# Performance work log

Hardware: AMD Instinct MI355X
Metric: run time of the kernel (lower is better)

## Reference

```python
import jax, jax.numpy as jnp
import numpy as np

BN_EPS = 1e-5
L2_EPS = 1e-12


def setup_inputs() -> dict:
    key = jax.random.key(0)
    k1, k2, k3 = jax.random.split(key, 3)
    B, N, D, K, G = 32, 2048, 512, 64, 16
    init_sc = 1.0 / np.sqrt(D)
    x = jax.random.normal(k1, (B, N, D), dtype=jnp.float32)
    clusters = init_sc * jax.random.normal(k2, (D, K + G), dtype=jnp.float32)
    clusters2 = init_sc * jax.random.normal(k3, (1, D, K), dtype=jnp.float32)
    bn_gamma = jnp.ones((K + G,), dtype=jnp.float32)
    bn_beta = jnp.zeros((K + G,), dtype=jnp.float32)
    return {"x": x, "clusters": clusters, "clusters2": clusters2,
            "bn_gamma": bn_gamma, "bn_beta": bn_beta}


def reference(x, clusters, clusters2, bn_gamma, bn_beta):
    B, N, D = x.shape
    K = clusters2.shape[-1]
    xf = x.reshape(B * N, D)
    # soft cluster assignment: [B*N, K+G]
    assn = xf @ clusters
    # BatchNorm1d (training-mode batch statistics, biased variance)
    mean = jnp.mean(assn, axis=0)
    var = jnp.var(assn, axis=0)
    assn = (assn - mean) * jax.lax.rsqrt(var + BN_EPS) * bn_gamma + bn_beta
    # softmax over clusters, then drop ghost clusters
    assn = jax.nn.softmax(assn, axis=1)[:, :K].reshape(B, N, K)
    # residual aggregation
    a_sum = jnp.sum(assn, axis=1, keepdims=True)          # [B, 1, K]
    a = a_sum * clusters2                                  # [B, D, K]
    vlad = jnp.einsum("bnk,bnd->bdk", assn, x) - a         # [B, D, K]
    # intra-normalization across feature dim D
    vlad = vlad / jnp.maximum(jnp.linalg.norm(vlad, axis=1, keepdims=True), L2_EPS)
    # flatten and global L2 normalization
    vlad = vlad.reshape(B, D * K)
    vlad = vlad / jnp.maximum(jnp.linalg.norm(vlad, axis=1, keepdims=True), L2_EPS)
    return vlad
```

## Files before the change

### kernel.cpp

```cpp
#include <hip/hip_runtime.h>
#include <hip/hip_bf16.h>
#include <stdint.h>

typedef __attribute__((ext_vector_type(8))) short short8;
typedef __attribute__((ext_vector_type(4))) float f32x4;

__device__ __forceinline__ float b2f(uint16_t u) {
  union { uint32_t i; float f; } v; v.i = ((uint32_t)u) << 16; return v.f;
}
__device__ __forceinline__ uint16_t f2b(float f) {
  uint32_t u = __float_as_uint(f);
  return (uint16_t)((u + 0x7FFFu + ((u >> 16) & 1u)) >> 16);
}
__device__ __forceinline__ uint32_t pk2(uint32_t lo, uint32_t hi) {
  return __builtin_amdgcn_perm(hi + 0x8000u, lo + 0x8000u, 0x07060302u);
}

__global__ void k0_prep(const float* __restrict__ clusters,
                        uint16_t* __restrict__ cB) {
  int gid = blockIdx.x * 256 + threadIdx.x;
  if (gid < 40960) {
    int i = gid & 7, chunk = gid >> 3;
    int lr = chunk & 15, q = (chunk >> 4) & 3, c5 = chunk >> 6;
    int n = c5 % 5, kk = c5 / 5;
    cB[gid] = f2b(clusters[(kk * 32 + q * 8 + i) * 80 + n * 16 + lr]);
  }
}

__global__ __launch_bounds__(256) void k1_gemm1(
    const float* __restrict__ x, const uint16_t* __restrict__ cB,
    float* __restrict__ raw, float* __restrict__ part) {
  __shared__ __align__(16) uint16_t lB[80 * 256];
  const int t = threadIdx.x;
  const int w = t >> 6, lane = t & 63, q = lane >> 4, lr = lane & 15;
  const int rbase = blockIdx.x * 128 + w * 32;

  f32x4 acc[2][5];
#pragma unroll
  for (int m = 0; m < 2; ++m)
#pragma unroll
    for (int n = 0; n < 5; ++n) acc[m][n] = 0.f;

  const float* xa = x + (size_t)(rbase + lr) * 512 + q * 8;

  for (int h = 0; h < 2; ++h) {
    if (h) __syncthreads();
#pragma unroll 2
    for (int idx = t; idx < 2560; idx += 256)
      *(uint4*)&lB[idx * 8] = ((const uint4*)cB)[h * 2560 + idx];
    __syncthreads();
#pragma unroll
    for (int kk8 = 0; kk8 < 8; ++kk8) {
      const int kk = h * 8 + kk8;
      short8 a[2], bf[5];
#pragma unroll
      for (int m = 0; m < 2; ++m) {
        uint4 u0 = *(const uint4*)(xa + (size_t)m * 16 * 512 + kk * 32);
        uint4 u1 = *(const uint4*)(xa + (size_t)m * 16 * 512 + kk * 32 + 4);
        union { short8 s; uint32_t u[4]; } av;
        av.u[0] = pk2(u0.x, u0.y); av.u[1] = pk2(u0.z, u0.w);
        av.u[2] = pk2(u1.x, u1.y); av.u[3] = pk2(u1.z, u1.w);
        a[m] = av.s;
      }
#pragma unroll
      for (int n = 0; n < 5; ++n)
        bf[n] = *(const short8*)&lB[(((kk8 * 5 + n) * 4 + q) * 16 + lr) * 8];
#pragma unroll
      for (int m = 0; m < 2; ++m)
#pragma unroll
        for (int n = 0; n < 5; ++n)
          acc[m][n] = __builtin_amdgcn_mfma_f32_16x16x32_bf16(a[m], bf[n], acc[m][n], 0, 0, 0);
    }
  }
  __syncthreads();

  float sums[5], sqs[5];
#pragma unroll
  for (int n = 0; n < 5; ++n) {
    float s = 0.f, qq = 0.f;
#pragma unroll
    for (int m = 0; m < 2; ++m) {
#pragma unroll
      for (int r = 0; r < 4; ++r) {
        float v = acc[m][n][r];
        s += v; qq += v * v;
        raw[(size_t)(rbase + m * 16 + q * 4 + r) * 80 + n * 16 + lr] = v;
      }
    }
    s += __shfl_xor(s, 16);  s += __shfl_xor(s, 32);
    qq += __shfl_xor(qq, 16); qq += __shfl_xor(qq, 32);
    sums[n] = s; sqs[n] = qq;
  }

  float* sf = (float*)lB;
  if (lane < 16) {
#pragma unroll
    for (int n = 0; n < 5; ++n) {
      sf[w * 160 + n * 16 + lr] = sums[n];
      sf[640 + w * 160 + n * 16 + lr] = sqs[n];
    }
  }
  __syncthreads();
  if (t < 160) {
    float a0 = sf[t] + sf[160 + t] + sf[320 + t] + sf[480 + t];
    float b0 = sf[640 + t] + sf[800 + t] + sf[960 + t] + sf[1120 + t];
    part[(size_t)blockIdx.x * 320 + t] = a0;
    part[(size_t)blockIdx.x * 320 + 160 + t] = b0;
  }
}

__global__ __launch_bounds__(64) void k2_stats(
    const float* __restrict__ part, const float* __restrict__ gamma,
    const float* __restrict__ beta, float* __restrict__ scsh,
    float* __restrict__ a_sum) {
  int c = blockIdx.x, t = threadIdx.x;
  int gid = c * 64 + t;
  if (gid < 2048) a_sum[gid] = 0.f;
  float s1 = 0.f, s2 = 0.f;
  for (int p = t; p < 512; p += 64) {
    s1 += part[(size_t)p * 320 + c];
    s2 += part[(size_t)p * 320 + 160 + c];
  }
#pragma unroll
  for (int o = 1; o < 64; o <<= 1) { s1 += __shfl_xor(s1, o); s2 += __shfl_xor(s2, o); }
  if (t == 0) {
    float mean = s1 * (1.f / 65536.f);
    float var = s2 * (1.f / 65536.f) - mean * mean;
    float sc = rsqrtf(var + 1e-5f) * gamma[c];
    scsh[c] = sc;
    scsh[80 + c] = beta[c] - mean * sc;
  }
}

__global__ __launch_bounds__(256) void k3_bnsoft(
    const float* __restrict__ raw, const float* __restrict__ scsh,
    uint16_t* __restrict__ pT, float* __restrict__ a_sum) {
  __shared__ float sc[80], sh[80];
  __shared__ __align__(16) uint16_t lpT[64 * 72];
  __shared__ float apart[256];
  const int t = threadIdx.x;
  if (t < 80) sc[t] = scsh[t];
  else if (t < 160) sh[t - 80] = scsh[t];
  __syncthreads();

  const int r = t >> 2, cg = t & 3;
  const float* rp = raw + ((size_t)blockIdx.x * 64 + r) * 80;
  const int cbase = cg * 20;

  float y[20];
#pragma unroll
  for (int j = 0; j < 20; j += 4) {
    float4 v = *(const float4*)(rp + cbase + j);
    y[j] = v.x; y[j + 1] = v.y; y[j + 2] = v.z; y[j + 3] = v.w;
  }
  float mx = -3.0e38f;
#pragma unroll
  for (int j = 0; j < 20; ++j) {
    int c = cbase + j;
    y[j] = y[j] * sc[c] + sh[c];
    mx = fmaxf(mx, y[j]);
  }
  mx = fmaxf(mx, __shfl_xor(mx, 1));
  mx = fmaxf(mx, __shfl_xor(mx, 2));
  float sum = 0.f;
#pragma unroll
  for (int j = 0; j < 20; ++j) { y[j] = __expf(y[j] - mx); sum += y[j]; }
  sum += __shfl_xor(sum, 1);
  sum += __shfl_xor(sum, 2);
  float inv = 1.0f / sum;
#pragma unroll
  for (int j = 0; j < 20; ++j) {
    int c = cbase + j;
    if (c < 64) lpT[c * 72 + r] = f2b(y[j] * inv);
  }
  __syncthreads();

  {
    int k = t >> 2, ng = t & 3;
    uint4 v0 = *(const uint4*)&lpT[k * 72 + ng * 16];
    uint4 v1 = *(const uint4*)&lpT[k * 72 + ng * 16 + 8];
    int b = blockIdx.x >> 5;
    int n0 = (blockIdx.x & 31) * 64;
    uint16_t* dst = pT + ((size_t)b * 64 + k) * 2048 + n0 + ng * 16;
    *(uint4*)dst = v0;
    *((uint4*)dst + 1) = v1;
    const uint16_t* pv = &lpT[k * 72 + ng * 16];
    float s = 0.f;
#pragma unroll
    for (int i = 0; i < 16; ++i) s += b2f(pv[i]);
    apart[k * 4 + ng] = s;
  }
  __syncthreads();
  if (t < 64) {
    float s = apart[t * 4] + apart[t * 4 + 1] + apart[t * 4 + 2] + apart[t * 4 + 3];
    atomicAdd(&a_sum[(blockIdx.x >> 5) * 64 + t], s);
  }
}

__global__ __launch_bounds__(256) void k4_gemm2(
    const float* __restrict__ x, const uint16_t* __restrict__ pT,
    float* __restrict__ vpart) {
  __shared__ __align__(16) uint16_t sx[2][64 * 40];
  __shared__ __align__(16) uint16_t sp[2][64 * 40];
  const int t = threadIdx.x;
  const int nb = blockIdx.x >> 8;
  const int b = (blockIdx.x >> 3) & 31;
  const int d0 = (blockIdx.x & 7) * 64;
  const int w = t >> 6, lane = t & 63, q = lane >> 4, lr = lane & 15;
  const int dl = w * 16 + lr;
  const int sw = ((dl >> 2) + (dl >> 4)) & 3;

  const int dd = t & 63, g = t >> 6;
  const int sg = ((dd >> 2) + (dd >> 4)) & 3;
  const int pk_ = t >> 2, pnq = t & 3;

  const float* xb = x + ((size_t)b * 2048 + (size_t)nb * 1024) * 512 + d0;
  const uint16_t* pb = pT + (size_t)b * 131072 + (size_t)nb * 1024;

  f32x4 acc[4];
#pragma unroll
  for (int j = 0; j < 4; ++j) acc[j] = 0.f;

  float xf[2][8];
  uint4 pf[2];

#define LOADC(c, si)                                                        \
  {                                                                         \
    const float* xc = xb + (size_t)(c) * 32 * 512;                          \
    _Pragma("unroll")                                                       \
    for (int jj = 0; jj < 8; ++jj)                                          \
      xf[si][jj] = xc[(size_t)(g * 8 + jj) * 512 + dd];                     \
    pf[si] = *(const uint4*)(pb + (size_t)pk_ * 2048 + (c) * 32 + pnq * 8); \
  }
#define STOREC(buf, si)                                                     \
  {                                                                         \
    uint16_t* xrow = &sx[buf][dd * 40 + (g ^ sg) * 8];                      \
    _Pragma("unroll")                                                       \
    for (int j = 0; j < 2; ++j) {                                           \
      *(uint32_t*)&xrow[j * 4] =                                            \
          pk2(__float_as_uint(xf[si][j * 4]), __float_as_uint(xf[si][j * 4 + 1])); \
      *(uint32_t*)&xrow[j * 4 + 2] =                                        \
          pk2(__float_as_uint(xf[si][j * 4 + 2]), __float_as_uint(xf[si][j * 4 + 3])); \
    }                                                                       \
    *(uint4*)&sp[buf][pk_ * 40 + pnq * 8] = pf[si];                         \
  }

  LOADC(0, 0)
  STOREC(0, 0)
  LOADC(1, 1)
  __syncthreads();

  for (int c = 0; c < 32; ++c) {
    const int cur = c & 1;
    if (c < 31) STOREC(cur ^ 1, (c + 1) & 1)
    if (c < 30) LOADC(c + 2, c & 1)
    const uint16_t* sxc = sx[cur];
    const uint16_t* spc = sp[cur];
    short8 af = *(const short8*)&sxc[dl * 40 + (q ^ sw) * 8];
#pragma unroll
    for (int j = 0; j < 4; ++j) {
      short8 bfj = *(const short8*)&spc[(j * 16 + lr) * 40 + q * 8];
      acc[j] = __builtin_amdgcn_mfma_f32_16x16x32_bf16(af, bfj, acc[j], 0, 0, 0);
    }
    __syncthreads();
  }
#undef LOADC
#undef STOREC

  float* vp = vpart + (size_t)nb * 1048576 + (size_t)b * 32768;
#pragma unroll
  for (int j = 0; j < 4; ++j)
#pragma unroll
    for (int r = 0; r < 4; ++r)
      vp[(size_t)(d0 + w * 16 + q * 4 + r) * 64 + j * 16 + lr] = acc[j][r];
}

__global__ __launch_bounds__(256) void k5a_ssq(
    const float* __restrict__ vpart, const float* __restrict__ a_sum,
    const float* __restrict__ c2, float* __restrict__ csq) {
  __shared__ float sred[256];
  const int t = threadIdx.x, b = blockIdx.x >> 4, dg = blockIdx.x & 15;
  const int k = t & 63, di = t >> 6;
  const float* v0 = vpart + (size_t)b * 32768;
  const float* v1 = v0 + 1048576;
  const float as = a_sum[b * 64 + k];
  float ssq = 0.f;
#pragma unroll
  for (int jj = 0; jj < 8; ++jj) {
    int i = (dg * 32 + di * 8 + jj) * 64 + k;
    float v = v0[i] + v1[i] - as * c2[i];
    ssq += v * v;
  }
  sred[di * 64 + k] = ssq;
  __syncthreads();
  if (t < 64) {
    csq[(size_t)blockIdx.x * 64 + t] =
        sred[t] + sred[64 + t] + sred[128 + t] + sred[192 + t];
  }
}

__global__ __launch_bounds__(64) void k5b_fin(
    const float* __restrict__ csq, float* __restrict__ linv,
    float* __restrict__ gscl) {
  const int t = threadIdx.x, b = blockIdx.x;
  float ssq = 0.f;
#pragma unroll
  for (int dg = 0; dg < 16; ++dg) ssq += csq[(size_t)(b * 16 + dg) * 64 + t];
  float iv = 1.0f / fmaxf(sqrtf(ssq), 1e-12f);
  linv[b * 64 + t] = iv;
  float contrib = ssq * iv * iv;
#pragma unroll
  for (int o = 1; o < 64; o <<= 1) contrib += __shfl_xor(contrib, o);
  if (t == 0) gscl[b] = 1.0f / fmaxf(sqrtf(contrib), 1e-12f);
}

__global__ __launch_bounds__(256) void k5c_norm(
    const float* __restrict__ vpart, const float* __restrict__ a_sum,
    const float* __restrict__ c2, const float* __restrict__ linv,
    const float* __restrict__ gscl, float* __restrict__ out) {
  __shared__ float lv[64], las[64];
  __shared__ float gs;
  const int t = threadIdx.x, b = blockIdx.x >> 4, seg = blockIdx.x & 15;
  if (t < 64) { lv[t] = linv[b * 64 + t]; las[t] = a_sum[b * 64 + t]; }
  if (t == 64) gs = gscl[b];
  __syncthreads();
  const float* v0 = vpart + (size_t)b * 32768;
  const float* v1 = v0 + 1048576;
  const float gg = gs;
#pragma unroll
  for (int u = 0; u < 2; ++u) {
    int i = seg * 2048 + u * 1024 + t * 4;
    int k0 = i & 63;
    float4 a = *(const float4*)(v0 + i);
    float4 bb = *(const float4*)(v1 + i);
    float4 cc = *(const float4*)(c2 + i);
    float4 o;
    o.x = (a.x + bb.x - las[k0 + 0] * cc.x) * lv[k0 + 0] * gg;
    o.y = (a.y + bb.y - las[k0 + 1] * cc.y) * lv[k0 + 1] * gg;
    o.z = (a.z + bb.z - las[k0 + 2] * cc.z) * lv[k0 + 2] * gg;
    o.w = (a.w + bb.w - las[k0 + 3] * cc.w) * lv[k0 + 3] * gg;
    *(float4*)&out[(size_t)b * 32768 + i] = o;
  }
}

extern "C" void kernel_launch(void* const* d_in, const int* in_sizes, int n_in,
                              void* d_out, int out_size, void* d_ws, size_t ws_size,
                              hipStream_t stream) {
  const float* x         = (const float*)d_in[0];
  const float* clusters  = (const float*)d_in[1];
  const float* clusters2 = (const float*)d_in[2];
  const float* gamma     = (const float*)d_in[3];
  const float* beta      = (const float*)d_in[4];
  float* out = (float*)d_out;
  char* ws = (char*)d_ws;

  uint16_t* cB = (uint16_t*)(ws + 0);
  float* part  = (float*)(ws + 81920);
  float* scsh  = (float*)(ws + 737280);
  float* a_sum = (float*)(ws + 737920);
  float* raw   = (float*)(ws + 746112);
  uint16_t* pT = (uint16_t*)(ws + 21717632);
  float* vpart = (float*)(ws + 30106240);
  float* csq   = (float*)(ws + 38494848);
  float* linv  = (float*)(ws + 38625920);
  float* gscl  = (float*)(ws + 38634112);

  hipLaunchKernelGGL(k0_prep,   dim3(160), dim3(256), 0, stream, clusters, cB);
  hipLaunchKernelGGL(k1_gemm1,  dim3(512), dim3(256), 0, stream, x, cB, raw, part);
  hipLaunchKernelGGL(k2_stats,  dim3(80),  dim3(64),  0, stream, part, gamma, beta, scsh, a_sum);
  hipLaunchKernelGGL(k3_bnsoft, dim3(1024),dim3(256), 0, stream, raw, scsh, pT, a_sum);
  hipLaunchKernelGGL(k4_gemm2,  dim3(512), dim3(256), 0, stream, x, pT, vpart);
  hipLaunchKernelGGL(k5a_ssq,   dim3(512), dim3(256), 0, stream, vpart, a_sum, clusters2, csq);
  hipLaunchKernelGGL(k5b_fin,   dim3(32),  dim3(64),  0, stream, csq, linv, gscl);
  hipLaunchKernelGGL(k5c_norm,  dim3(512), dim3(256), 0, stream, vpart, a_sum, clusters2, linv, gscl, out);
}
```

Baseline: 257.9 us.

## Fuse BN-softmax into second GEMM and restructure reduction pipeline

Merges the batchnorm/softmax kernel with the aggregation GEMM, so softmax probabilities are computed per tile straight into shared memory instead of being written out as a transposed bf16 buffer and read back. The GEMM now splits N into 8 segments with larger 256-wide D tiles, and a new reduction kernel sums the 8 partial results into a full buffer. The cluster-sum atomics are replaced by per-segment partials. The first GEMM loads all of cB into LDS once, and the stats partials are transposed so reads are coalesced. The cost is a larger vpart (8 partials) and an extra vfull write/read.

```diff
diff --git a/kernel.cpp b/kernel.cpp
--- a/kernel.cpp
+++ b/kernel.cpp
@@ -30,11 +30,18 @@
 __global__ __launch_bounds__(256) void k1_gemm1(
     const float* __restrict__ x, const uint16_t* __restrict__ cB,
     float* __restrict__ raw, float* __restrict__ part) {
-  __shared__ __align__(16) uint16_t lB[80 * 256];
+  __shared__ __align__(16) uint16_t lB[80 * 512];
   const int t = threadIdx.x;
   const int w = t >> 6, lane = t & 63, q = lane >> 4, lr = lane & 15;
   const int rbase = blockIdx.x * 128 + w * 32;
 
+  {
+    const uint4* src = (const uint4*)cB;
+#pragma unroll 4
+    for (int it = 0; it < 20; ++it)
+      *(uint4*)&lB[(it * 256 + t) * 8] = src[it * 256 + t];
+  }
+
   f32x4 acc[2][5];
 #pragma unroll
   for (int m = 0; m < 2; ++m)
@@ -42,35 +49,28 @@
     for (int n = 0; n < 5; ++n) acc[m][n] = 0.f;
 
   const float* xa = x + (size_t)(rbase + lr) * 512 + q * 8;
-
-  for (int h = 0; h < 2; ++h) {
-    if (h) __syncthreads();
-#pragma unroll 2
-    for (int idx = t; idx < 2560; idx += 256)
-      *(uint4*)&lB[idx * 8] = ((const uint4*)cB)[h * 2560 + idx];
-    __syncthreads();
-#pragma unroll
-    for (int kk8 = 0; kk8 < 8; ++kk8) {
-      const int kk = h * 8 + kk8;
-      short8 a[2], bf[5];
-#pragma unroll
-      for (int m = 0; m < 2; ++m) {
-        uint4 u0 = *(const uint4*)(xa + (size_t)m * 16 * 512 + kk * 32);
-        uint4 u1 = *(const uint4*)(xa + (size_t)m * 16 * 512 + kk * 32 + 4);
-        union { short8 s; uint32_t u[4]; } av;
-        av.u[0] = pk2(u0.x, u0.y); av.u[1] = pk2(u0.z, u0.w);
-        av.u[2] = pk2(u1.x, u1.y); av.u[3] = pk2(u1.z, u1.w);
-        a[m] = av.s;
-      }
+  __syncthreads();
+
+#pragma unroll 8
+  for (int kk = 0; kk < 16; ++kk) {
+    short8 a[2], bf[5];
+#pragma unroll
+    for (int m = 0; m < 2; ++m) {
+      uint4 u0 = *(const uint4*)(xa + (size_t)m * 16 * 512 + kk * 32);
+      uint4 u1 = *(const uint4*)(xa + (size_t)m * 16 * 512 + kk * 32 + 4);
+      union { short8 s; uint32_t u[4]; } av;
+      av.u[0] = pk2(u0.x, u0.y); av.u[1] = pk2(u0.z, u0.w);
+      av.u[2] = pk2(u1.x, u1.y); av.u[3] = pk2(u1.z, u1.w);
+      a[m] = av.s;
+    }
+#pragma unroll
+    for (int n = 0; n < 5; ++n)
+      bf[n] = *(const short8*)&lB[(((kk * 5 + n) * 4 + q) * 16 + lr) * 8];
+#pragma unroll
+    for (int m = 0; m < 2; ++m)
 #pragma unroll
       for (int n = 0; n < 5; ++n)
-        bf[n] = *(const short8*)&lB[(((kk8 * 5 + n) * 4 + q) * 16 + lr) * 8];
-#pragma unroll
-      for (int m = 0; m < 2; ++m)
-#pragma unroll
-        for (int n = 0; n < 5; ++n)
-          acc[m][n] = __builtin_amdgcn_mfma_f32_16x16x32_bf16(a[m], bf[n], acc[m][n], 0, 0, 0);
-    }
+        acc[m][n] = __builtin_amdgcn_mfma_f32_16x16x32_bf16(a[m], bf[n], acc[m][n], 0, 0, 0);
   }
   __syncthreads();
 
@@ -104,23 +104,20 @@
   if (t < 160) {
     float a0 = sf[t] + sf[160 + t] + sf[320 + t] + sf[480 + t];
     float b0 = sf[640 + t] + sf[800 + t] + sf[960 + t] + sf[1120 + t];
-    part[(size_t)blockIdx.x * 320 + t] = a0;
-    part[(size_t)blockIdx.x * 320 + 160 + t] = b0;
+    part[(size_t)t * 512 + blockIdx.x] = a0;
+    part[(size_t)(160 + t) * 512 + blockIdx.x] = b0;
   }
 }
 
 __global__ __launch_bounds__(64) void k2_stats(
     const float* __restrict__ part, const float* __restrict__ gamma,
-    const float* __restrict__ beta, float* __restrict__ scsh,
-    float* __restrict__ a_sum) {
+    const float* __restrict__ beta, float* __restrict__ scsh) {
   int c = blockIdx.x, t = threadIdx.x;
-  int gid = c * 64 + t;
-  if (gid < 2048) a_sum[gid] = 0.f;
+  const float* p1 = part + (size_t)c * 512;
+  const float* p2 = part + (size_t)(160 + c) * 512;
   float s1 = 0.f, s2 = 0.f;
-  for (int p = t; p < 512; p += 64) {
-    s1 += part[(size_t)p * 320 + c];
-    s2 += part[(size_t)p * 320 + 160 + c];
-  }
+#pragma unroll
+  for (int p = 0; p < 512; p += 64) { s1 += p1[p + t]; s2 += p2[p + t]; }
 #pragma unroll
   for (int o = 1; o < 64; o <<= 1) { s1 += __shfl_xor(s1, o); s2 += __shfl_xor(s2, o); }
   if (t == 0) {
@@ -132,163 +129,180 @@
   }
 }
 
-__global__ __launch_bounds__(256) void k3_bnsoft(
-    const float* __restrict__ raw, const float* __restrict__ scsh,
-    uint16_t* __restrict__ pT, float* __restrict__ a_sum) {
+__global__ __launch_bounds__(256, 2) void k34_fused(
+    const float* __restrict__ x, const float* __restrict__ raw_,
+    const float* __restrict__ scsh, float* __restrict__ vpart,
+    float* __restrict__ apart) {
+  __shared__ __align__(16) uint16_t sx[2][256 * 40];
+  __shared__ __align__(16) uint16_t sp[2][64 * 40];
   __shared__ float sc[80], sh[80];
-  __shared__ __align__(16) uint16_t lpT[64 * 72];
-  __shared__ float apart[256];
+  __shared__ float ared[4 * 64];
+
   const int t = threadIdx.x;
+  const int b = blockIdx.x >> 4;
+  const int s = (blockIdx.x >> 1) & 7;
+  const int dh = blockIdx.x & 1;
+  const int w = t >> 6, lane = t & 63, q = lane >> 4, lr = lane & 15;
+
+  const int dd = t;
+  const int sg = ((dd >> 2) + (dd >> 4)) & 3;
+  const int r_ = t >> 3, cg = t & 7;
+  const int kk_ = t & 63, ng = t >> 6;
+
   if (t < 80) sc[t] = scsh[t];
   else if (t < 160) sh[t - 80] = scsh[t];
-  __syncthreads();
-
-  const int r = t >> 2, cg = t & 3;
-  const float* rp = raw + ((size_t)blockIdx.x * 64 + r) * 80;
-  const int cbase = cg * 20;
-
-  float y[20];
-#pragma unroll
-  for (int j = 0; j < 20; j += 4) {
-    float4 v = *(const float4*)(rp + cbase + j);
-    y[j] = v.x; y[j + 1] = v.y; y[j + 2] = v.z; y[j + 3] = v.w;
-  }
-  float mx = -3.0e38f;
-#pragma unroll
-  for (int j = 0; j < 20; ++j) {
-    int c = cbase + j;
-    y[j] = y[j] * sc[c] + sh[c];
-    mx = fmaxf(mx, y[j]);
-  }
-  mx = fmaxf(mx, __shfl_xor(mx, 1));
-  mx = fmaxf(mx, __shfl_xor(mx, 2));
-  float sum = 0.f;
-#pragma unroll
-  for (int j = 0; j < 20; ++j) { y[j] = __expf(y[j] - mx); sum += y[j]; }
-  sum += __shfl_xor(sum, 1);
-  sum += __shfl_xor(sum, 2);
-  float inv = 1.0f / sum;
-#pragma unroll
-  for (int j = 0; j < 20; ++j) {
-    int c = cbase + j;
-    if (c < 64) lpT[c * 72 + r] = f2b(y[j] * inv);
-  }
-  __syncthreads();
-
-  {
-    int k = t >> 2, ng = t & 3;
-    uint4 v0 = *(const uint4*)&lpT[k * 72 + ng * 16];
-    uint4 v1 = *(const uint4*)&lpT[k * 72 + ng * 16 + 8];
-    int b = blockIdx.x >> 5;
-    int n0 = (blockIdx.x & 31) * 64;
-    uint16_t* dst = pT + ((size_t)b * 64 + k) * 2048 + n0 + ng * 16;
-    *(uint4*)dst = v0;
-    *((uint4*)dst + 1) = v1;
-    const uint16_t* pv = &lpT[k * 72 + ng * 16];
-    float s = 0.f;
-#pragma unroll
-    for (int i = 0; i < 16; ++i) s += b2f(pv[i]);
-    apart[k * 4 + ng] = s;
-  }
-  __syncthreads();
-  if (t < 64) {
-    float s = apart[t * 4] + apart[t * 4 + 1] + apart[t * 4 + 2] + apart[t * 4 + 3];
-    atomicAdd(&a_sum[(blockIdx.x >> 5) * 64 + t], s);
-  }
-}
-
-__global__ __launch_bounds__(256) void k4_gemm2(
-    const float* __restrict__ x, const uint16_t* __restrict__ pT,
-    float* __restrict__ vpart) {
-  __shared__ __align__(16) uint16_t sx[2][64 * 40];
-  __shared__ __align__(16) uint16_t sp[2][64 * 40];
-  const int t = threadIdx.x;
-  const int nb = blockIdx.x >> 8;
-  const int b = (blockIdx.x >> 3) & 31;
-  const int d0 = (blockIdx.x & 7) * 64;
-  const int w = t >> 6, lane = t & 63, q = lane >> 4, lr = lane & 15;
-  const int dl = w * 16 + lr;
-  const int sw = ((dl >> 2) + (dl >> 4)) & 3;
-
-  const int dd = t & 63, g = t >> 6;
-  const int sg = ((dd >> 2) + (dd >> 4)) & 3;
-  const int pk_ = t >> 2, pnq = t & 3;
-
-  const float* xb = x + ((size_t)b * 2048 + (size_t)nb * 1024) * 512 + d0;
-  const uint16_t* pb = pT + (size_t)b * 131072 + (size_t)nb * 1024;
-
-  f32x4 acc[4];
-#pragma unroll
-  for (int j = 0; j < 4; ++j) acc[j] = 0.f;
-
-  float xf[2][8];
-  uint4 pf[2];
-
-#define LOADC(c, si)                                                        \
-  {                                                                         \
-    const float* xc = xb + (size_t)(c) * 32 * 512;                          \
-    _Pragma("unroll")                                                       \
-    for (int jj = 0; jj < 8; ++jj)                                          \
-      xf[si][jj] = xc[(size_t)(g * 8 + jj) * 512 + dd];                     \
-    pf[si] = *(const uint4*)(pb + (size_t)pk_ * 2048 + (c) * 32 + pnq * 8); \
-  }
-#define STOREC(buf, si)                                                     \
-  {                                                                         \
-    uint16_t* xrow = &sx[buf][dd * 40 + (g ^ sg) * 8];                      \
-    _Pragma("unroll")                                                       \
-    for (int j = 0; j < 2; ++j) {                                           \
-      *(uint32_t*)&xrow[j * 4] =                                            \
-          pk2(__float_as_uint(xf[si][j * 4]), __float_as_uint(xf[si][j * 4 + 1])); \
-      *(uint32_t*)&xrow[j * 4 + 2] =                                        \
-          pk2(__float_as_uint(xf[si][j * 4 + 2]), __float_as_uint(xf[si][j * 4 + 3])); \
-    }                                                                       \
-    *(uint4*)&sp[buf][pk_ * 40 + pnq * 8] = pf[si];                         \
-  }
-
-  LOADC(0, 0)
-  STOREC(0, 0)
-  LOADC(1, 1)
-  __syncthreads();
-
-  for (int c = 0; c < 32; ++c) {
+
+  const float* xb = x + ((size_t)b * 2048 + (size_t)s * 256) * 512 + dh * 256;
+  const float* rawb = raw_ + ((size_t)b * 2048 + (size_t)s * 256) * 80;
+
+  f32x4 acc[4][4];
+#pragma unroll
+  for (int m = 0; m < 4; ++m)
+#pragma unroll
+    for (int j = 0; j < 4; ++j) acc[m][j] = 0.f;
+
+  float xf[32], yf[10];
+  float asum = 0.f;
+
+#define XLOAD(c)                                                          \
+  {                                                                       \
+    const float* xc = xb + (size_t)(c) * 32 * 512 + dd;                   \
+    _Pragma("unroll")                                                     \
+    for (int j = 0; j < 32; ++j) xf[j] = xc[(size_t)j * 512];             \
+  }
+#define RLOAD(c)                                                          \
+  {                                                                       \
+    const float* rc = rawb + (size_t)((c) * 32 + r_) * 80 + cg * 10;      \
+    _Pragma("unroll")                                                     \
+    for (int j = 0; j < 5; ++j) {                                         \
+      float2 v2 = *(const float2*)(rc + j * 2);                           \
+      yf[2 * j] = v2.x; yf[2 * j + 1] = v2.y;                             \
+    }                                                                     \
+  }
+#define XSTORE(buf)                                                       \
+  {                                                                       \
+    _Pragma("unroll")                                                     \
+    for (int g = 0; g < 4; ++g) {                                         \
+      union { uint4 u; uint32_t w4[4]; } pv;                              \
+      _Pragma("unroll")                                                   \
+      for (int h = 0; h < 4; ++h)                                         \
+        pv.w4[h] = pk2(__float_as_uint(xf[g * 8 + h * 2]),                \
+                       __float_as_uint(xf[g * 8 + h * 2 + 1]));           \
+      *(uint4*)&sx[buf][dd * 40 + ((g ^ sg) << 3)] = pv.u;                \
+    }                                                                     \
+  }
+#define SOFTMAX(buf)                                                      \
+  {                                                                       \
+    float yy[10]; float mx = -3.0e38f;                                    \
+    _Pragma("unroll")                                                     \
+    for (int j = 0; j < 10; ++j) {                                        \
+      int cc = cg * 10 + j;                                               \
+      yy[j] = yf[j] * sc[cc] + sh[cc];                                    \
+      mx = fmaxf(mx, yy[j]);                                              \
+    }                                                                     \
+    mx = fmaxf(mx, __shfl_xor(mx, 1));                                    \
+    mx = fmaxf(mx, __shfl_xor(mx, 2));                                    \
+    mx = fmaxf(mx, __shfl_xor(mx, 4));                                    \
+    float sum = 0.f;                                                      \
+    _Pragma("unroll")                                                     \
+    for (int j = 0; j < 10; ++j) { yy[j] = __expf(yy[j] - mx); sum += yy[j]; } \
+    sum += __shfl_xor(sum, 1);                                            \
+    sum += __shfl_xor(sum, 2);                                            \
+    sum += __shfl_xor(sum, 4);                                            \
+    float inv = 1.0f / sum;                                               \
+    _Pragma("unroll")                                                     \
+    for (int j = 0; j < 10; ++j) {                                        \
+      int cc = cg * 10 + j;                                               \
+      if (cc < 64) sp[buf][cc * 40 + r_] = f2b(yy[j] * inv);              \
+    }                                                                     \
+  }
+#define GEMM(buf)                                                         \
+  {                                                                       \
+    const uint16_t* sxc = sx[buf];                                        \
+    const uint16_t* spc = sp[buf];                                        \
+    short8 bfr[4];                                                        \
+    _Pragma("unroll")                                                     \
+    for (int j = 0; j < 4; ++j)                                           \
+      bfr[j] = *(const short8*)&spc[(j * 16 + lr) * 40 + (q << 3)];       \
+    _Pragma("unroll")                                                     \
+    for (int m = 0; m < 4; ++m) {                                         \
+      int row = w * 64 + m * 16 + lr;                                     \
+      int swr = ((row >> 2) + (row >> 4)) & 3;                            \
+      short8 af = *(const short8*)&sxc[row * 40 + ((q ^ swr) << 3)];      \
+      _Pragma("unroll")                                                   \
+      for (int j = 0; j < 4; ++j)                                         \
+        acc[m][j] = __builtin_amdgcn_mfma_f32_16x16x32_bf16(af, bfr[j], acc[m][j], 0, 0, 0); \
+    }                                                                     \
+    union { uint4 u; uint16_t us[8]; } pv;                                \
+    pv.u = *(const uint4*)&spc[kk_ * 40 + (ng << 3)];                     \
+    _Pragma("unroll")                                                     \
+    for (int i = 0; i < 8; ++i) asum += b2f(pv.us[i]);                    \
+  }
+
+  XLOAD(0) RLOAD(0)
+  __syncthreads();
+  XSTORE(0) SOFTMAX(0)
+  XLOAD(1) RLOAD(1)
+  __syncthreads();
+
+  for (int c = 0; c < 8; ++c) {
     const int cur = c & 1;
-    if (c < 31) STOREC(cur ^ 1, (c + 1) & 1)
-    if (c < 30) LOADC(c + 2, c & 1)
-    const uint16_t* sxc = sx[cur];
-    const uint16_t* spc = sp[cur];
-    short8 af = *(const short8*)&sxc[dl * 40 + (q ^ sw) * 8];
-#pragma unroll
-    for (int j = 0; j < 4; ++j) {
-      short8 bfj = *(const short8*)&spc[(j * 16 + lr) * 40 + q * 8];
-      acc[j] = __builtin_amdgcn_mfma_f32_16x16x32_bf16(af, bfj, acc[j], 0, 0, 0);
+    GEMM(cur)
+    __syncthreads();
+    if (c < 7) {
+      XSTORE(cur ^ 1) SOFTMAX(cur ^ 1)
+      if (c < 6) { XLOAD(c + 2) RLOAD(c + 2) }
+      __syncthreads();
     }
-    __syncthreads();
-  }
-#undef LOADC
-#undef STOREC
-
-  float* vp = vpart + (size_t)nb * 1048576 + (size_t)b * 32768;
-#pragma unroll
-  for (int j = 0; j < 4; ++j)
-#pragma unroll
-    for (int r = 0; r < 4; ++r)
-      vp[(size_t)(d0 + w * 16 + q * 4 + r) * 64 + j * 16 + lr] = acc[j][r];
-}
-
-__global__ __launch_bounds__(256) void k5a_ssq(
-    const float* __restrict__ vpart, const float* __restrict__ a_sum,
-    const float* __restrict__ c2, float* __restrict__ csq) {
+  }
+#undef XLOAD
+#undef RLOAD
+#undef XSTORE
+#undef SOFTMAX
+#undef GEMM
+
+  ared[ng * 64 + kk_] = asum;
+  __syncthreads();
+  if (dh == 0 && t < 64) {
+    float a = ared[t] + ared[64 + t] + ared[128 + t] + ared[192 + t];
+    apart[((size_t)b * 8 + s) * 64 + t] = a;
+  }
+
+  float* vp = vpart + ((size_t)s * 32 + b) * 32768;
+#pragma unroll
+  for (int m = 0; m < 4; ++m)
+#pragma unroll
+    for (int j = 0; j < 4; ++j)
+#pragma unroll
+      for (int r2 = 0; r2 < 4; ++r2)
+        vp[(size_t)(dh * 256 + w * 64 + m * 16 + q * 4 + r2) * 64 + j * 16 + lr] =
+            acc[m][j][r2];
+}
+
+__global__ __launch_bounds__(256) void k5a_red(
+    const float* __restrict__ vpart, const float* __restrict__ apart,
+    const float* __restrict__ c2, float* __restrict__ vfull,
+    float* __restrict__ csq) {
+  __shared__ float las[64];
   __shared__ float sred[256];
   const int t = threadIdx.x, b = blockIdx.x >> 4, dg = blockIdx.x & 15;
+  if (t < 64) {
+    float a = 0.f;
+#pragma unroll
+    for (int s = 0; s < 8; ++s) a += apart[((size_t)b * 8 + s) * 64 + t];
+    las[t] = a;
+  }
+  __syncthreads();
   const int k = t & 63, di = t >> 6;
-  const float* v0 = vpart + (size_t)b * 32768;
-  const float* v1 = v0 + 1048576;
-  const float as = a_sum[b * 64 + k];
   float ssq = 0.f;
 #pragma unroll
   for (int jj = 0; jj < 8; ++jj) {
-    int i = (dg * 32 + di * 8 + jj) * 64 + k;
-    float v = v0[i] + v1[i] - as * c2[i];
+    int d = dg * 32 + di * 8 + jj;
+    size_t i = (size_t)d * 64 + k;
+    float v = -las[k] * c2[i];
+#pragma unroll
+    for (int s = 0; s < 8; ++s) v += vpart[((size_t)s * 32 + b) * 32768 + i];
+    vfull[(size_t)b * 32768 + i] = v;
     ssq += v * v;
   }
   sred[di * 64 + k] = ssq;
@@ -315,30 +329,25 @@
 }
 
 __global__ __launch_bounds__(256) void k5c_norm(
-    const float* __restrict__ vpart, const float* __restrict__ a_sum,
-    const float* __restrict__ c2, const float* __restrict__ linv,
+    const float* __restrict__ vfull, const float* __restrict__ linv,
     const float* __restrict__ gscl, float* __restrict__ out) {
-  __shared__ float lv[64], las[64];
+  __shared__ float lv[64];
   __shared__ float gs;
   const int t = threadIdx.x, b = blockIdx.x >> 4, seg = blockIdx.x & 15;
-  if (t < 64) { lv[t] = linv[b * 64 + t]; las[t] = a_sum[b * 64 + t]; }
+  if (t < 64) lv[t] = linv[b * 64 + t];
   if (t == 64) gs = gscl[b];
   __syncthreads();
-  const float* v0 = vpart + (size_t)b * 32768;
-  const float* v1 = v0 + 1048576;
   const float gg = gs;
 #pragma unroll
   for (int u = 0; u < 2; ++u) {
     int i = seg * 2048 + u * 1024 + t * 4;
     int k0 = i & 63;
-    float4 a = *(const float4*)(v0 + i);
-    float4 bb = *(const float4*)(v1 + i);
-    float4 cc = *(const float4*)(c2 + i);
+    float4 a = *(const float4*)(vfull + (size_t)b * 32768 + i);
     float4 o;
-    o.x = (a.x + bb.x - las[k0 + 0] * cc.x) * lv[k0 + 0] * gg;
-    o.y = (a.y + bb.y - las[k0 + 1] * cc.y) * lv[k0 + 1] * gg;
-    o.z = (a.z + bb.z - las[k0 + 2] * cc.z) * lv[k0 + 2] * gg;
-    o.w = (a.w + bb.w - las[k0 + 3] * cc.w) * lv[k0 + 3] * gg;
+    o.x = a.x * lv[k0 + 0] * gg;
+    o.y = a.y * lv[k0 + 1] * gg;
+    o.z = a.z * lv[k0 + 2] * gg;
+    o.w = a.w * lv[k0 + 3] * gg;
     *(float4*)&out[(size_t)b * 32768 + i] = o;
   }
 }
@@ -357,20 +366,19 @@
   uint16_t* cB = (uint16_t*)(ws + 0);
   float* part  = (float*)(ws + 81920);
   float* scsh  = (float*)(ws + 737280);
-  float* a_sum = (float*)(ws + 737920);
-  float* raw   = (float*)(ws + 746112);
-  uint16_t* pT = (uint16_t*)(ws + 21717632);
-  float* vpart = (float*)(ws + 30106240);
-  float* csq   = (float*)(ws + 38494848);
-  float* linv  = (float*)(ws + 38625920);
-  float* gscl  = (float*)(ws + 38634112);
+  float* raw   = (float*)(ws + 737920);
+  float* vpart = (float*)(ws + 21709440);
+  float* vfull = (float*)(ws + 55263872);
+  float* apart = (float*)(ws + 59458176);
+  float* csq   = (float*)(ws + 59523712);
+  float* linv  = (float*)(ws + 59654784);
+  float* gscl  = (float*)(ws + 59662976);
 
   hipLaunchKernelGGL(k0_prep,   dim3(160), dim3(256), 0, stream, clusters, cB);
   hipLaunchKernelGGL(k1_gemm1,  dim3(512), dim3(256), 0, stream, x, cB, raw, part);
-  hipLaunchKernelGGL(k2_stats,  dim3(80),  dim3(64),  0, stream, part, gamma, beta, scsh, a_sum);
-  hipLaunchKernelGGL(k3_bnsoft, dim3(1024),dim3(256), 0, stream, raw, scsh, pT, a_sum);
-  hipLaunchKernelGGL(k4_gemm2,  dim3(512), dim3(256), 0, stream, x, pT, vpart);
-  hipLaunchKernelGGL(k5a_ssq,   dim3(512), dim3(256), 0, stream, vpart, a_sum, clusters2, csq);
+  hipLaunchKernelGGL(k2_stats,  dim3(80),  dim3(64),  0, stream, part, gamma, beta, scsh);
+  hipLaunchKernelGGL(k34_fused, dim3(512), dim3(256), 0, stream, x, raw, scsh, vpart, apart);
+  hipLaunchKernelGGL(k5a_red,   dim3(512), dim3(256), 0, stream, vpart, apart, clusters2, vfull, csq);
   hipLaunchKernelGGL(k5b_fin,   dim3(32),  dim3(64),  0, stream, csq, linv, gscl);
-  hipLaunchKernelGGL(k5c_norm,  dim3(512), dim3(256), 0, stream, vpart, a_sum, clusters2, linv, gscl, out);
-}
+  hipLaunchKernelGGL(k5c_norm,  dim3(512), dim3(256), 0, stream, vfull, linv, gscl, out);
+}
```

Measured after the change: 249.2 us. -3.4%, faster.
